# Kernel tuning notes

Measured on AMD Instinct MI355X. Metric: run time of the kernel, lower is better.

Reference implementation:

```python
import jax, jax.numpy as jnp
import numpy as np

B, N, C = 8, 16384, 256

def setup_inputs() -> dict:
    key = jax.random.key(0)
    ks = jax.random.split(key, 5)
    scale = 1.0 / np.sqrt(C)
    return {
        "x_in": jax.random.normal(ks[0], (B, N, C), dtype=jnp.float32),
        "Wq": jax.random.normal(ks[1], (C, C), dtype=jnp.float32) * scale,
        "bq": jax.random.normal(ks[2], (C,), dtype=jnp.float32) * scale,
        "Wk": jax.random.normal(ks[3], (C, C), dtype=jnp.float32) * scale,
        "bk": jax.random.normal(ks[4], (C,), dtype=jnp.float32) * scale,
    }

def reference(x_in, Wq, bq, Wk, bk):
    b, n, c = x_in.shape
    # Faithful to torch: reshape (NOT transpose) to [B, C, N]
    x = x_in.reshape(b, c, n)
    # 1x1 Conv1d == per-position linear over channel dim
    Q = jnp.einsum('oc,bcn->bon', Wq, x) + bq[None, :, None]  # [B,C,N]
    K = jnp.einsum('oc,bcn->bon', Wk, x) + bk[None, :, None]  # [B,C,N]
    # Q @ K^T over length axis -> channel-channel scores [B,C,C]
    scores = jnp.einsum('bcn,bdn->bcd', Q, K)
    c_c = jax.nn.softmax(scores, axis=-1)
    # x_in @ c_c + residual -> [B,N,C]
    return jnp.einsum('bnc,bcd->bnd', x_in, c_c) + x_in
```

## Files before the change

### kernel.cpp

```cpp
#include <hip/hip_runtime.h>

#define Bn 8
#define Nn 16384
#define Cn 256
#define NC 32
#define CHUNK 512
#define NSTG 8

typedef __attribute__((ext_vector_type(4)))  float f32x4;
typedef __attribute__((ext_vector_type(16))) float f32x16;
typedef __attribute__((ext_vector_type(8)))  __bf16 bf16x8;
typedef __attribute__((ext_vector_type(8)))  _Float16 f16x8;
typedef __attribute__((ext_vector_type(8)))  unsigned short u16x8;

static __device__ __forceinline__ unsigned short f2bf(float f) {
    unsigned int u = __float_as_uint(f);
    u += 0x7fff + ((u >> 16) & 1);
    return (unsigned short)(u >> 16);
}
static __device__ __forceinline__ unsigned short f2h(float f) {
    return __builtin_bit_cast(unsigned short, (_Float16)f);
}
static __device__ __forceinline__ f32x16 mfma16h(u16x8 a, u16x8 b, f32x16 c) {
    return __builtin_amdgcn_mfma_f32_32x32x16_f16(
        __builtin_bit_cast(f16x8, a), __builtin_bit_cast(f16x8, b), c, 0, 0, 0);
}
static __device__ __forceinline__ f32x16 mfma16b(u16x8 a, u16x8 b, f32x16 c) {
    return __builtin_amdgcn_mfma_f32_32x32x16_bf16(
        __builtin_bit_cast(bf16x8, a), __builtin_bit_cast(bf16x8, b), c, 0, 0, 0);
}

__global__ __launch_bounds__(256, 2) void k_gram(
    const float* __restrict__ x, float* __restrict__ gpart,
    float* __restrict__ spart) {
  const int blk  = blockIdx.x;
  const int half = blk & 1;
  const int ck   = (blk >> 1) & (NC - 1);
  const int b    = blk >> 6;
  const float* xb = x + (size_t)b * Cn * Nn + (size_t)ck * CHUNK;

  __shared__ __align__(16) char smem[32768];

  const int t    = threadIdx.x;
  const int lane = t & 63;
  const int w    = t >> 6;
  const int ln   = lane & 31;
  const int kh   = lane >> 5;

  const int rt = t >> 4;
  const int c4 = t & 15;

  f32x16 acc[4][2];
#pragma unroll
  for (int m = 0; m < 4; ++m)
#pragma unroll
    for (int n = 0; n < 2; ++n)
#pragma unroll
      for (int i = 0; i < 16; ++i) acc[m][n][i] = 0.f;

  float srow[16];
#pragma unroll
  for (int j = 0; j < 16; ++j) srow[j] = 0.f;

  const float* xrow = xb + (size_t)rt * Nn + c4 * 4;

  for (int s = 0; s < NSTG; ++s) {
#pragma unroll
    for (int j = 0; j < 16; ++j) {
      f32x4 v = *(const f32x4*)(xrow + (size_t)j * (16 * Nn) + s * 64);
      srow[j] += v.x + v.y + v.z + v.w;
      ushort4 h = make_ushort4(f2h(v.x), f2h(v.y), f2h(v.z), f2h(v.w));
      int row = rt + 16 * j;
      *(ushort4*)(smem + row * 128 + 16 * ((c4 >> 1) ^ (row & 7)) + (c4 & 1) * 8) = h;
    }
    __syncthreads();
#pragma unroll
    for (int ks = 0; ks < 4; ++ks) {
      const int sl = ks * 2 + kh;
      u16x8 A[4], Bv[2];
#pragma unroll
      for (int m = 0; m < 4; ++m) {
        int r = half * 128 + m * 32 + ln;
        A[m] = *(const u16x8*)(smem + r * 128 + 16 * (sl ^ (r & 7)));
      }
#pragma unroll
      for (int n = 0; n < 2; ++n) {
        int r = w * 64 + n * 32 + ln;
        Bv[n] = *(const u16x8*)(smem + r * 128 + 16 * (sl ^ (r & 7)));
      }
#pragma unroll
      for (int m = 0; m < 4; ++m)
#pragma unroll
        for (int n = 0; n < 2; ++n)
          acc[m][n] = mfma16h(A[m], Bv[n], acc[m][n]);
    }
    __syncthreads();
  }

#pragma unroll
  for (int j = 0; j < 16; ++j) {
    float v = srow[j];
    v += __shfl_xor(v, 1);
    v += __shfl_xor(v, 2);
    v += __shfl_xor(v, 4);
    v += __shfl_xor(v, 8);
    if (c4 == 0 && half == 0)
      spart[(size_t)(b * NC + ck) * Cn + rt + 16 * j] = v;
  }

  float* gp = gpart + (size_t)(b * NC + ck) * (Cn * Cn);
#pragma unroll
  for (int m = 0; m < 4; ++m)
#pragma unroll
    for (int n = 0; n < 2; ++n)
#pragma unroll
      for (int r2 = 0; r2 < 16; ++r2) {
        int row = half * 128 + m * 32 + (r2 & 3) + 8 * (r2 >> 2) + 4 * kh;
        int col = w * 64 + n * 32 + ln;
        gp[row * Cn + col] = acc[m][n][r2];
      }
}

__global__ __launch_bounds__(256) void k_misc(
    const float* __restrict__ spart, const float* __restrict__ wk,
    const float* __restrict__ bk, float* __restrict__ sv,
    float* __restrict__ wkT, float* __restrict__ kN) {
  const int bb = blockIdx.x, t = threadIdx.x;
  __shared__ float s_l[256];
  float a = 0.f;
  for (int ck = 0; ck < NC; ++ck) a += spart[(size_t)(bb * NC + ck) * Cn + t];
  sv[bb * Cn + t] = a;
  s_l[t] = a;
#pragma unroll
  for (int j = 0; j < 32; ++j) {
    int k = bb * 32 + j;
    wkT[k * Cn + t] = wk[t * Cn + k];
  }
  __syncthreads();
  float k2 = 0.f;
  for (int c = 0; c < 256; ++c) k2 += wk[t * Cn + c] * s_l[c];
  kN[bb * Cn + t] = k2 + 16384.f * bk[t];
}

__global__ __launch_bounds__(256) void k_gk(
    const float* __restrict__ gpart, const float* __restrict__ sv,
    const float* __restrict__ wkT, const float* __restrict__ bk,
    float* __restrict__ GK) {
  const int b = blockIdx.x >> 5, tile = blockIdx.x & 31;
  const int r0 = tile * 8, t = threadIdx.x;
  __shared__ float g_l[8][256];

  float a[8];
#pragma unroll
  for (int j = 0; j < 8; ++j) a[j] = 0.f;
  const float* gp = gpart + (size_t)b * NC * 65536 + r0 * 256 + t;
  for (int ck = 0; ck < NC; ++ck) {
#pragma unroll
    for (int j = 0; j < 8; ++j) a[j] += gp[(size_t)ck * 65536 + j * 256];
  }
#pragma unroll
  for (int j = 0; j < 8; ++j) g_l[j][t] = a[j];
  __syncthreads();

  float acc[8];
#pragma unroll
  for (int r = 0; r < 8; ++r) acc[r] = 0.f;
  for (int k0 = 0; k0 < 256; k0 += 4) {
    float w0 = wkT[(k0 + 0) * 256 + t];
    float w1 = wkT[(k0 + 1) * 256 + t];
    float w2 = wkT[(k0 + 2) * 256 + t];
    float w3 = wkT[(k0 + 3) * 256 + t];
#pragma unroll
    for (int r = 0; r < 8; ++r) {
      f32x4 gv = *(const f32x4*)(&g_l[r][k0]);
      acc[r] += gv.x * w0 + gv.y * w1 + gv.z * w2 + gv.w * w3;
    }
  }
  float bkt = bk[t];
#pragma unroll
  for (int r = 0; r < 8; ++r) {
    float svr = sv[b * 256 + r0 + r];
    GK[((size_t)b * 256 + r0 + r) * 256 + t] = acc[r] + svr * bkt;
  }
}

__global__ __launch_bounds__(256) void k_scores(
    const float* __restrict__ wq, const float* __restrict__ GK,
    const float* __restrict__ bq, const float* __restrict__ kN,
    unsigned short* __restrict__ ccB) {
  const int b    = blockIdx.x >> 5;
  const int tile = blockIdx.x & 31;
  const int c0   = tile * 8;
  const int t    = threadIdx.x;

  __shared__ float wq_l[8][256];
  __shared__ float sc_l[8][256];
  __shared__ unsigned short cct_l[256][8];

#pragma unroll
  for (int j = 0; j < 8; ++j) wq_l[j][t] = wq[(c0 + j) * Cn + t];
  __syncthreads();

  float acc[8];
#pragma unroll
  for (int r = 0; r < 8; ++r) acc[r] = 0.f;
  for (int k0 = 0; k0 < 256; k0 += 4) {
    float g0 = GK[((size_t)b * 256 + k0 + 0) * 256 + t];
    float g1 = GK[((size_t)b * 256 + k0 + 1) * 256 + t];
    float g2 = GK[((size_t)b * 256 + k0 + 2) * 256 + t];
    float g3 = GK[((size_t)b * 256 + k0 + 3) * 256 + t];
#pragma unroll
    for (int r = 0; r < 8; ++r) {
      f32x4 qv = *(const f32x4*)(&wq_l[r][k0]);
      acc[r] += qv.x * g0 + qv.y * g1 + qv.z * g2 + qv.w * g3;
    }
  }
  float kNt = kN[b * 256 + t];
#pragma unroll
  for (int r = 0; r < 8; ++r) sc_l[r][t] = acc[r] + bq[c0 + r] * kNt;
  __syncthreads();

  const int r = t >> 5, sub = t & 31;
  float v[8];
#pragma unroll
  for (int j = 0; j < 8; ++j) v[j] = sc_l[r][sub + 32 * j];
  float mx = v[0];
#pragma unroll
  for (int j = 1; j < 8; ++j) mx = fmaxf(mx, v[j]);
#pragma unroll
  for (int msk = 16; msk >= 1; msk >>= 1) mx = fmaxf(mx, __shfl_xor(mx, msk, 32));
  float se = 0.f;
#pragma unroll
  for (int j = 0; j < 8; ++j) { v[j] = __expf(v[j] - mx); se += v[j]; }
#pragma unroll
  for (int msk = 16; msk >= 1; msk >>= 1) se += __shfl_xor(se, msk, 32);
  float inv = 1.f / se;
#pragma unroll
  for (int j = 0; j < 8; ++j) {
    int d = sub + 32 * j;
    float cc = v[j] * inv + ((d == c0 + r) ? 1.f : 0.f);
    cct_l[d][r] = f2bf(cc);
  }
  __syncthreads();
  *(uint4*)(ccB + (size_t)b * 65536 + (size_t)(tile * 256 + t) * 8) =
      *(const uint4*)(&cct_l[t][0]);
}

__global__ __launch_bounds__(256, 4) void k_out(
    const float* __restrict__ x, const unsigned short* __restrict__ ccB,
    float* __restrict__ out) {
  const int blk = blockIdx.x;
  const int b  = blk >> 8;
  const int n0 = (blk & 255) * 64;
  const float* xb = x + (size_t)b * Nn * Cn + (size_t)n0 * Cn;
  const unsigned short* cb = ccB + (size_t)b * 65536;
  float* ob = out + (size_t)b * Nn * Cn + (size_t)n0 * Cn;

  __shared__ __align__(16) char smem[32768];

  const int t    = threadIdx.x;
  const int lane = t & 63;
  const int w    = t >> 6;
  const int ln = lane & 31;
  const int kh = lane >> 5;

  f32x16 acc[2][2];
#pragma unroll
  for (int m = 0; m < 2; ++m)
#pragma unroll
    for (int n = 0; n < 2; ++n)
#pragma unroll
      for (int i = 0; i < 16; ++i) acc[m][n][i] = 0.f;

#pragma unroll
  for (int i = 0; i < 16; ++i) {
    int fi = i * 256 + t;
    f32x4 v = *(const f32x4*)(xb + (size_t)fi * 4);
    int row = fi >> 6, c = fi & 63;
    ushort4 hv = make_ushort4(f2bf(v.x), f2bf(v.y), f2bf(v.z), f2bf(v.w));
    *(ushort4*)(smem + row * 512 + ((c * 8) ^ ((row & 31) << 4))) = hv;
  }
  __syncthreads();

#pragma unroll
  for (int ks = 0; ks < 16; ++ks) {
    u16x8 A[2], Bv[2];
    const int g = ks * 2 + kh;
#pragma unroll
    for (int m = 0; m < 2; ++m) {
      int row = m * 32 + ln;
      A[m] = *(const u16x8*)(smem + row * 512 + ((g * 16) ^ ((row & 31) << 4)));
    }
#pragma unroll
    for (int n = 0; n < 2; ++n) {
      int d = w * 64 + n * 32 + ln;
      Bv[n] = *(const u16x8*)(cb + (size_t)g * 2048 + (size_t)d * 8);
    }
#pragma unroll
    for (int m = 0; m < 2; ++m)
#pragma unroll
      for (int n = 0; n < 2; ++n)
        acc[m][n] = mfma16b(A[m], Bv[n], acc[m][n]);
  }

#pragma unroll
  for (int m = 0; m < 2; ++m)
#pragma unroll
    for (int n = 0; n < 2; ++n)
#pragma unroll
      for (int r2 = 0; r2 < 16; ++r2) {
        int row = m * 32 + (r2 & 3) + 8 * (r2 >> 2) + 4 * kh;
        int col = w * 64 + n * 32 + ln;
        ob[(size_t)row * Cn + col] = acc[m][n][r2];
      }
}

extern "C" void kernel_launch(void* const* d_in, const int* in_sizes, int n_in,
                              void* d_out, int out_size, void* d_ws, size_t ws_size,
                              hipStream_t stream) {
  const float* x  = (const float*)d_in[0];
  const float* wq = (const float*)d_in[1];
  const float* bq = (const float*)d_in[2];
  const float* wk = (const float*)d_in[3];
  const float* bk = (const float*)d_in[4];
  float* out = (float*)d_out;

  float* gpart = (float*)d_ws;
  float* spart = gpart + (size_t)Bn * NC * 65536;
  float* sv    = spart + (size_t)Bn * NC * 256;
  float* wkT   = sv + (size_t)Bn * 256;
  float* kN    = wkT + 65536;
  float* GK    = kN + (size_t)Bn * 256;
  unsigned short* ccB = (unsigned short*)(GK + (size_t)Bn * 65536);

  hipLaunchKernelGGL(k_gram,   dim3(Bn * NC * 2), dim3(256), 0, stream, x, gpart, spart);
  hipLaunchKernelGGL(k_misc,   dim3(Bn),          dim3(256), 0, stream, spart, wk, bk, sv, wkT, kN);
  hipLaunchKernelGGL(k_gk,     dim3(Bn * 32),     dim3(256), 0, stream, gpart, sv, wkT, bk, GK);
  hipLaunchKernelGGL(k_scores, dim3(Bn * 32),     dim3(256), 0, stream, wq, GK, bq, kN, ccB);
  hipLaunchKernelGGL(k_out,    dim3(Bn * 256),    dim3(256), 0, stream, x, ccB, out);
}
```

Measured before the change: 161.3 us.

## Restructure gram kernel with register prefetch, double-buffered LDS and 512 threads

The gram kernel now prefetches the next stage's global loads into registers while the current stage is converted and written to one of two LDS buffers. This removes one barrier per stage, and each block works through 16 stages of 32 columns. Blocks grow to 8 waves, each computing a 64x64 output tile. The LDS layout changes from an XOR swizzle to a padded 80-byte row stride, and each block starts its column sweep at a rotated offset to spread concurrent global reads across addresses. The aim is to overlap HBM latency with MFMA work and raise occupancy, at the cost of higher register pressure and fewer MFMAs per LDS read.

```diff
diff --git a/kernel.cpp b/kernel.cpp
--- a/kernel.cpp
+++ b/kernel.cpp
@@ -5,7 +5,7 @@
 #define Cn 256
 #define NC 32
 #define CHUNK 512
-#define NSTG 8
+#define NSTG 16
 
 typedef __attribute__((ext_vector_type(4)))  float f32x4;
 typedef __attribute__((ext_vector_type(16))) float f32x16;
@@ -30,7 +30,7 @@
         __builtin_bit_cast(bf16x8, a), __builtin_bit_cast(bf16x8, b), c, 0, 0, 0);
 }
 
-__global__ __launch_bounds__(256, 2) void k_gram(
+__global__ __launch_bounds__(512, 4) void k_gram(
     const float* __restrict__ x, float* __restrict__ gpart,
     float* __restrict__ spart) {
   const int blk  = blockIdx.x;
@@ -38,85 +38,98 @@
   const int ck   = (blk >> 1) & (NC - 1);
   const int b    = blk >> 6;
   const float* xb = x + (size_t)b * Cn * Nn + (size_t)ck * CHUNK;
-
-  __shared__ __align__(16) char smem[32768];
+  const int rot  = (2 * ck + half) & (NSTG - 1);
+
+  __shared__ __align__(16) char smem[2 * 20480];
 
   const int t    = threadIdx.x;
   const int lane = t & 63;
   const int w    = t >> 6;
+  const int wm   = w & 1;
+  const int wn   = w >> 1;
   const int ln   = lane & 31;
   const int kh   = lane >> 5;
 
-  const int rt = t >> 4;
-  const int c4 = t & 15;
-
-  f32x16 acc[4][2];
-#pragma unroll
-  for (int m = 0; m < 4; ++m)
+  const int rt = t >> 3;
+  const int c4 = t & 7;
+
+  f32x16 acc[2][2];
+#pragma unroll
+  for (int m = 0; m < 2; ++m)
 #pragma unroll
     for (int n = 0; n < 2; ++n)
 #pragma unroll
       for (int i = 0; i < 16; ++i) acc[m][n][i] = 0.f;
 
-  float srow[16];
-#pragma unroll
-  for (int j = 0; j < 16; ++j) srow[j] = 0.f;
-
-  const float* xrow = xb + (size_t)rt * Nn + c4 * 4;
+  float srow[4] = {0.f, 0.f, 0.f, 0.f};
+  const float* xrt = xb + (size_t)rt * Nn + c4 * 4;
+
+  f32x4 ld[4];
+  {
+    const int sp = rot;
+#pragma unroll
+    for (int j = 0; j < 4; ++j)
+      ld[j] = *(const f32x4*)(xrt + (size_t)j * (64 * Nn) + sp * 32);
+  }
 
   for (int s = 0; s < NSTG; ++s) {
-#pragma unroll
-    for (int j = 0; j < 16; ++j) {
-      f32x4 v = *(const f32x4*)(xrow + (size_t)j * (16 * Nn) + s * 64);
+    char* buf = smem + (s & 1) * 20480;
+#pragma unroll
+    for (int j = 0; j < 4; ++j) {
+      f32x4 v = ld[j];
       srow[j] += v.x + v.y + v.z + v.w;
       ushort4 h = make_ushort4(f2h(v.x), f2h(v.y), f2h(v.z), f2h(v.w));
-      int row = rt + 16 * j;
-      *(ushort4*)(smem + row * 128 + 16 * ((c4 >> 1) ^ (row & 7)) + (c4 & 1) * 8) = h;
+      int row = rt + 64 * j;
+      *(ushort4*)(buf + row * 80 + c4 * 8) = h;
+    }
+    if (s + 1 < NSTG) {
+      const int sp = (s + 1 + rot) & (NSTG - 1);
+#pragma unroll
+      for (int j = 0; j < 4; ++j)
+        ld[j] = *(const f32x4*)(xrt + (size_t)j * (64 * Nn) + sp * 32);
     }
     __syncthreads();
 #pragma unroll
-    for (int ks = 0; ks < 4; ++ks) {
+    for (int ks = 0; ks < 2; ++ks) {
       const int sl = ks * 2 + kh;
-      u16x8 A[4], Bv[2];
-#pragma unroll
-      for (int m = 0; m < 4; ++m) {
-        int r = half * 128 + m * 32 + ln;
-        A[m] = *(const u16x8*)(smem + r * 128 + 16 * (sl ^ (r & 7)));
+      u16x8 A[2], Bv[2];
+#pragma unroll
+      for (int m = 0; m < 2; ++m) {
+        int r = half * 128 + wm * 64 + m * 32 + ln;
+        A[m] = *(const u16x8*)(buf + r * 80 + sl * 16);
       }
 #pragma unroll
       for (int n = 0; n < 2; ++n) {
-        int r = w * 64 + n * 32 + ln;
-        Bv[n] = *(const u16x8*)(smem + r * 128 + 16 * (sl ^ (r & 7)));
+        int r = wn * 64 + n * 32 + ln;
+        Bv[n] = *(const u16x8*)(buf + r * 80 + sl * 16);
       }
 #pragma unroll
-      for (int m = 0; m < 4; ++m)
+      for (int m = 0; m < 2; ++m)
 #pragma unroll
         for (int n = 0; n < 2; ++n)
           acc[m][n] = mfma16h(A[m], Bv[n], acc[m][n]);
     }
-    __syncthreads();
-  }
-
-#pragma unroll
-  for (int j = 0; j < 16; ++j) {
+  }
+
+#pragma unroll
+  for (int j = 0; j < 4; ++j) {
     float v = srow[j];
     v += __shfl_xor(v, 1);
     v += __shfl_xor(v, 2);
     v += __shfl_xor(v, 4);
-    v += __shfl_xor(v, 8);
     if (c4 == 0 && half == 0)
-      spart[(size_t)(b * NC + ck) * Cn + rt + 16 * j] = v;
+      spart[(size_t)(b * NC + ck) * Cn + rt + 64 * j] = v;
   }
 
   float* gp = gpart + (size_t)(b * NC + ck) * (Cn * Cn);
 #pragma unroll
-  for (int m = 0; m < 4; ++m)
+  for (int m = 0; m < 2; ++m)
 #pragma unroll
     for (int n = 0; n < 2; ++n)
 #pragma unroll
       for (int r2 = 0; r2 < 16; ++r2) {
-        int row = half * 128 + m * 32 + (r2 & 3) + 8 * (r2 >> 2) + 4 * kh;
-        int col = w * 64 + n * 32 + ln;
+        int row = half * 128 + wm * 64 + m * 32 + (r2 & 3) + 8 * (r2 >> 2) + 4 * kh;
+        int col = wn * 64 + n * 32 + ln;
         gp[row * Cn + col] = acc[m][n][r2];
       }
 }
@@ -333,7 +346,7 @@
   float* GK    = kN + (size_t)Bn * 256;
   unsigned short* ccB = (unsigned short*)(GK + (size_t)Bn * 65536);
 
-  hipLaunchKernelGGL(k_gram,   dim3(Bn * NC * 2), dim3(256), 0, stream, x, gpart, spart);
+  hipLaunchKernelGGL(k_gram,   dim3(Bn * NC * 2), dim3(512), 0, stream, x, gpart, spart);
   hipLaunchKernelGGL(k_misc,   dim3(Bn),          dim3(256), 0, stream, spart, wk, bk, sv, wkT, kN);
   hipLaunchKernelGGL(k_gk,     dim3(Bn * 32),     dim3(256), 0, stream, gpart, sv, wkT, bk, GK);
   hipLaunchKernelGGL(k_scores, dim3(Bn * 32),     dim3(256), 0, stream, wq, GK, bq, kN, ccB);
```

Result: faster. 156.6 us (-2.9%).
